# Kernel tuning notes

Hardware: AMD Instinct MI355X
Metric: run time of the kernel (lower is better)

The kernel has to match this reference:

```python
import jax, jax.numpy as jnp
import numpy as np

H = 64
VOCAB = 64
NUM_PAIRS = 6
ENERGY_THRESHOLD = 0.4
LN_EPS = 1e-5


def setup_inputs() -> dict:
    key = jax.random.key(0)
    ks = jax.random.split(key, 16)
    B, L = 256, 2048
    s = 0.05
    return {
        "x": jax.random.randint(ks[0], (B, L), 0, VOCAB),
        "embed": jax.random.normal(ks[1], (VOCAB, H), jnp.float32) * s,
        "W1": jax.random.normal(ks[2], (2 * H, H), jnp.float32) * s,
        "b1": jnp.zeros((2 * H,), jnp.float32),
        "W2": jax.random.normal(ks[3], (H, 2 * H), jnp.float32) * s,
        "b2": jnp.zeros((H,), jnp.float32),
        "ln_g": jnp.ones((H,), jnp.float32),
        "ln_b": jnp.zeros((H,), jnp.float32),
        "Wk": jax.random.normal(ks[4], (H, H), jnp.float32) * s,
        "Wv": jax.random.normal(ks[5], (H, H), jnp.float32) * s,
        "Wq": jax.random.normal(ks[6], (H, H), jnp.float32) * s,
        "Wr": jax.random.normal(ks[7], (H, H), jnp.float32) * s,
        "alpha": jnp.float32(0.5),
        "Wout": jax.random.normal(ks[8], (VOCAB, H), jnp.float32) * s,
        "bout": jnp.zeros((VOCAB,), jnp.float32),
    }


def _layernorm(x, g, b):
    mu = jnp.mean(x, axis=-1, keepdims=True)
    var = jnp.var(x, axis=-1, keepdims=True)
    return (x - mu) * jax.lax.rsqrt(var + LN_EPS) * g + b


def _encoder(x, embed, W1, b1, W2, b2, ln_g, ln_b):
    h = embed[x]                                  # [B, L, H]
    ff = jax.nn.relu(h @ W1.T + b1) @ W2.T + b2   # [B, L, H]
    return _layernorm(h + ff, ln_g, ln_b)


def _forward(x, embed, W1, b1, W2, b2, ln_g, ln_b, Wk, Wv, Wq, Wr, alpha, Wout, bout):
    h = _encoder(x, embed, W1, b1, W2, b2, ln_g, ln_b)  # [B, L, H]
    B, L, _ = h.shape

    def step(M, h_t):  # M: [B, H, H], h_t: [B, H]
        k = h_t @ Wk.T
        k = k / jnp.maximum(jnp.linalg.norm(k, axis=-1, keepdims=True), 1e-12)
        v = h_t @ Wv.T
        pred = jnp.einsum("bij,bj->bi", M, k)
        delta = v - pred
        gate = (jnp.linalg.norm(delta, axis=-1) >
                ENERGY_THRESHOLD * jnp.linalg.norm(v, axis=-1)).astype(M.dtype)
        M = M + gate[:, None, None] * delta[:, :, None] * k[:, None, :]
        return M, None

    M0 = jnp.zeros((B, H, H), h.dtype)
    M, _ = jax.lax.scan(step, M0, jnp.swapaxes(h, 0, 1))  # scan over L

    q = h[:, -1, :] @ Wq.T                 # [B, H]
    slots = jnp.swapaxes(M, 1, 2)          # [B, H, H]
    k_s = min(NUM_PAIRS + 2, H)
    norms = jnp.linalg.norm(slots, axis=-1)            # [B, H]
    _, topk_i = jax.lax.top_k(norms, k_s)              # [B, k_s]
    sel = jnp.take_along_axis(slots, topk_i[:, :, None], axis=1)  # [B, k_s, H]
    q_r = q @ Wr.T
    attn = jax.nn.softmax(jnp.einsum("bkh,bh->bk", sel, q_r) / jnp.sqrt(jnp.float32(H)), axis=-1)
    retro_ctx = jnp.einsum("bk,bkh->bh", attn, sel)    # [B, H]
    m_ctx = jnp.einsum("bij,bj->bi", M, q)             # [B, H]
    a = jax.nn.sigmoid(alpha)
    mixed = jax.nn.relu(a * retro_ctx + (1.0 - a) * m_ctx)
    return mixed @ Wout.T + bout           # [B, VOCAB]


def reference(x, embed, W1, b1, W2, b2, ln_g, ln_b, Wk, Wv, Wq, Wr, alpha, Wout, bout):
    return _forward(x, embed, W1, b1, W2, b2, ln_g, ln_b, Wk, Wv, Wq, Wr, alpha, Wout, bout)
```

## Files before the change

kernel.cpp:

```cpp
#include <hip/hip_runtime.h>
#include <math.h>

#define H 64
#define VOCABN 64
#define LSEQ 2048
#define LN_EPS 1e-5f

template <int CTRL>
__device__ __forceinline__ float dpp_add(float x) {
  return x + __int_as_float(__builtin_amdgcn_update_dpp(
      0, __float_as_int(x), CTRL, 0xF, 0xF, true));
}

__device__ __forceinline__ float wave_allsum(float x) {
  x = dpp_add<0xB1>(x);
  x = dpp_add<0x4E>(x);
  x = dpp_add<0x141>(x);
  x = dpp_add<0x140>(x);
  x += __shfl_xor(x, 16, 64);
  x += __shfl_xor(x, 32, 64);
  return x;
}

__device__ __forceinline__ float reduce_to_lane63(float x) {
  x = dpp_add<0x111>(x);
  x = dpp_add<0x112>(x);
  x = dpp_add<0x114>(x);
  x = dpp_add<0x118>(x);
  x = dpp_add<0x142>(x);
  x = dpp_add<0x143>(x);
  return x;
}

__global__ __launch_bounds__(64) void tables_kernel(
    const float* __restrict__ embed, const float* __restrict__ W1, const float* __restrict__ b1,
    const float* __restrict__ W2, const float* __restrict__ b2,
    const float* __restrict__ ln_g, const float* __restrict__ ln_b,
    const float* __restrict__ Wk, const float* __restrict__ Wv,
    float* __restrict__ Htab, float* __restrict__ Ktab, float* __restrict__ Vtab,
    float* __restrict__ nvtab)
{
  __shared__ float hs[H];
  __shared__ float ff1[2 * H];
  __shared__ float lns[H];
  const int c = blockIdx.x;
  const int i = threadIdx.x;

  float e = embed[c * H + i];
  hs[i] = e;
  __syncthreads();

  float r1 = b1[i], r2 = b1[i + H];
  for (int j = 0; j < H; ++j) {
    float hj = hs[j];
    r1 = fmaf(W1[i * H + j], hj, r1);
    r2 = fmaf(W1[(i + H) * H + j], hj, r2);
  }
  ff1[i]     = fmaxf(r1, 0.f);
  ff1[i + H] = fmaxf(r2, 0.f);
  __syncthreads();

  float o = b2[i];
  for (int m = 0; m < 2 * H; ++m) o = fmaf(W2[i * 2 * H + m], ff1[m], o);
  float y = e + o;

  float mu  = wave_allsum(y) * (1.f / H);
  float d   = y - mu;
  float var = wave_allsum(d * d) * (1.f / H);
  float ln  = d * (1.f / sqrtf(var + LN_EPS)) * ln_g[i] + ln_b[i];
  lns[i] = ln;
  __syncthreads();
  Htab[c * H + i] = ln;

  float k = 0.f, v = 0.f;
  for (int j = 0; j < H; ++j) {
    float lj = lns[j];
    k = fmaf(Wk[i * H + j], lj, k);
    v = fmaf(Wv[i * H + j], lj, v);
  }
  float nk = sqrtf(wave_allsum(k * k));
  Ktab[c * H + i] = k / fmaxf(nk, 1e-12f);
  Vtab[c * H + i] = v;
  float nv = sqrtf(wave_allsum(v * v));
  if (i == 0) nvtab[c] = 0.4f * nv;
}

__global__ __launch_bounds__(256, 1) void scan_kernel(
    const int* __restrict__ x, const float* __restrict__ Htab,
    const float* __restrict__ Ktab, const float* __restrict__ Vtab,
    const float* __restrict__ nvtab,
    const float* __restrict__ Wq, const float* __restrict__ Wr,
    const float* __restrict__ alpha, const float* __restrict__ Wout,
    const float* __restrict__ bout, float* __restrict__ out)
{
  __shared__ float4 Kl4[VOCABN * H / 4];
  __shared__ float4 Vl4[VOCABN * H / 4];
  __shared__ float4 Gl4[VOCABN * H / 4];
  __shared__ float4 Rl4[VOCABN * H / 4];
  __shared__ int4   xl4[LSEQ / 4];
  __shared__ float  thl[VOCABN];
  __shared__ float  hbuf[H];
  __shared__ float  qbuf[H];
  __shared__ float  mbuf[H];
  float* Kl = (float*)Kl4;
  float* Vl = (float*)Vl4;
  float* Gl = (float*)Gl4;
  float* Rl = (float*)Rl4;
  int*   xl = (int*)xl4;

  const int b    = blockIdx.x;
  const int tid  = threadIdx.x;
  const int lane = tid & 63;
  const int wid  = tid >> 6;

  {
    const float4* Kg = (const float4*)Ktab;
    const float4* Vg = (const float4*)Vtab;
    for (int q = tid; q < VOCABN * H / 4; q += 256) {
      float4 vq = Vg[q];
      Kl4[q] = Kg[q]; Vl4[q] = vq; Rl4[q] = vq;
    }
    const int4* xg = (const int4*)(x + b * LSEQ);
    for (int q = tid; q < LSEQ / 4; q += 256) xl4[q] = xg[q];
    if (tid < VOCABN) thl[tid] = nvtab[tid];
  }
  __syncthreads();

  {
    float4 kr[16];
#pragma unroll
    for (int q = 0; q < 16; ++q) kr[q] = Kl4[lane * 16 + q];
    for (int r = 0; r < 16; ++r) {
      const int c2 = wid * 16 + r;
      const float4* kp2 = (const float4*)(Kl + c2 * H);
      float a0 = 0.f, a1 = 0.f, a2 = 0.f, a3 = 0.f;
#pragma unroll
      for (int q = 0; q < 16; ++q) {
        float4 kq = kp2[q];
        a0 = fmaf(kr[q].x, kq.x, a0);
        a1 = fmaf(kr[q].y, kq.y, a1);
        a2 = fmaf(kr[q].z, kq.z, a2);
        a3 = fmaf(kr[q].w, kq.w, a3);
      }
      Gl[c2 * H + lane] = (a0 + a1) + (a2 + a3);
    }
  }
  __syncthreads();

  float4 Mw[4];
#pragma unroll
  for (int q = 0; q < 4; ++q) Mw[q] = make_float4(0.f, 0.f, 0.f, 0.f);

  int   c0 = xl[0], c1 = xl[1];
  float rv  = Rl[c0 * H + lane];
  float rvn = Rl[c1 * H + lane];
  float th0 = thl[c0], th1 = thl[c1];

  for (int t = 0; t < LSEQ; ++t) {
    const int ix2 = (t + 2 < LSEQ) ? t + 2 : LSEQ - 1;
    const int c2  = xl[ix2];
    float rb2  = Rl[c2 * H + lane];
    float th2v = thl[c2];
    float g01  = Gl[c0 * H + c1];
    float g02  = Gl[c0 * H + c2];

    float nd2 = reduce_to_lane63(rv * rv);
    float nds = sqrtf(__int_as_float(__builtin_amdgcn_readlane(__float_as_int(nd2), 63)));
    float thu = __int_as_float(__builtin_amdgcn_readfirstlane(__float_as_int(th0)));

    if (nds > thu) {
      const float delta = rv;
      rvn = fmaf(-g01, delta, rvn);
      rb2 = fmaf(-g02, delta, rb2);
      __syncthreads();
      const float4* gp = ((const float4*)(Gl + c0 * H)) + wid * 4;
      float4 ga = gp[0], gb = gp[1], gc = gp[2], gd = gp[3];
      float gs[16] = {ga.x, ga.y, ga.z, ga.w, gb.x, gb.y, gb.z, gb.w,
                      gc.x, gc.y, gc.z, gc.w, gd.x, gd.y, gd.z, gd.w};
#pragma unroll
      for (int r = 0; r < 16; ++r) {
        const int cc = wid * 16 + r;
        Rl[cc * H + lane] = fmaf(-gs[r], delta, Rl[cc * H + lane]);
      }
      const float4* kp = ((const float4*)(Kl + c0 * H)) + wid * 4;
#pragma unroll
      for (int q = 0; q < 4; ++q) {
        float4 k4 = kp[q];
        Mw[q].x = fmaf(delta, k4.x, Mw[q].x);
        Mw[q].y = fmaf(delta, k4.y, Mw[q].y);
        Mw[q].z = fmaf(delta, k4.z, Mw[q].z);
        Mw[q].w = fmaf(delta, k4.w, Mw[q].w);
      }
      __syncthreads();
    }
    rv = rvn; rvn = rb2; c0 = c1; c1 = c2; th0 = th1; th1 = th2v;
  }

  __syncthreads();
#pragma unroll
  for (int r = 0; r < 4; ++r) {
    const int jb = wid * 16 + r * 4;
    float4 m = Mw[r];
    Vl[(jb + 0) * H + lane] = m.x;
    Vl[(jb + 1) * H + lane] = m.y;
    Vl[(jb + 2) * H + lane] = m.z;
    Vl[(jb + 3) * H + lane] = m.w;
    Kl[lane * H + jb + 0] = m.x;
    Kl[lane * H + jb + 1] = m.y;
    Kl[lane * H + jb + 2] = m.z;
    Kl[lane * H + jb + 3] = m.w;
  }
  __syncthreads();

  if (wid == 0) {
    const int clast = xl[LSEQ - 1];
    hbuf[lane] = Htab[clast * H + lane];

    float qi = 0.f;
    for (int j = 0; j < H; ++j) qi = fmaf(Wq[lane * H + j], hbuf[j], qi);
    qbuf[lane] = qi;

    float qri = 0.f;
    for (int j = 0; j < H; ++j) qri = fmaf(Wr[lane * H + j], qbuf[j], qri);

    float n2 = 0.f;
    for (int i2 = 0; i2 < H; ++i2) { float m = Kl[i2 * H + lane]; n2 = fmaf(m, m, n2); }

    const int KS = 8;
    int idxs[KS];
    float nloc = n2;
#pragma unroll
    for (int k = 0; k < KS; ++k) {
      float v = nloc; int idx = lane;
#pragma unroll
      for (int s = 1; s < 64; s <<= 1) {
        float ov = __shfl_xor(v, s, 64);
        int   oi = __shfl_xor(idx, s, 64);
        if (ov > v || (ov == v && oi < idx)) { v = ov; idx = oi; }
      }
      idxs[k] = idx;
      if (lane == idx) nloc = -1.f;
    }

    float sel[KS], lg[KS];
#pragma unroll
    for (int k = 0; k < KS; ++k) {
      float s = Vl[idxs[k] * H + lane];
      sel[k] = s;
      lg[k] = wave_allsum(s * qri) * 0.125f;
    }
    float lmax = lg[0];
#pragma unroll
    for (int k = 1; k < KS; ++k) lmax = fmaxf(lmax, lg[k]);
    float esum = 0.f, retro = 0.f;
#pragma unroll
    for (int k = 0; k < KS; ++k) {
      float e = expf(lg[k] - lmax);
      esum += e;
      retro = fmaf(e, sel[k], retro);
    }
    retro /= esum;

    float mc = 0.f;
    for (int j = 0; j < H; ++j) mc = fmaf(Vl[j * H + lane], qbuf[j], mc);

    float a = 1.f / (1.f + expf(-alpha[0]));
    float mixed = fmaxf(fmaf(a, retro, (1.f - a) * mc), 0.f);
    mbuf[lane] = mixed;

    float oo = bout[lane];
    for (int i2 = 0; i2 < H; ++i2) oo = fmaf(Wout[lane * H + i2], mbuf[i2], oo);
    out[b * VOCABN + lane] = oo;
  }
}

extern "C" void kernel_launch(void* const* d_in, const int* in_sizes, int n_in,
                              void* d_out, int out_size, void* d_ws, size_t ws_size,
                              hipStream_t stream) {
  const int*   x     = (const int*)d_in[0];
  const float* embed = (const float*)d_in[1];
  const float* W1    = (const float*)d_in[2];
  const float* b1    = (const float*)d_in[3];
  const float* W2    = (const float*)d_in[4];
  const float* b2    = (const float*)d_in[5];
  const float* ln_g  = (const float*)d_in[6];
  const float* ln_b  = (const float*)d_in[7];
  const float* Wk    = (const float*)d_in[8];
  const float* Wv    = (const float*)d_in[9];
  const float* Wq    = (const float*)d_in[10];
  const float* Wr    = (const float*)d_in[11];
  const float* alpha = (const float*)d_in[12];
  const float* Wout  = (const float*)d_in[13];
  const float* bout  = (const float*)d_in[14];
  float* out = (float*)d_out;

  const int B = in_sizes[0] / LSEQ;

  float* ws    = (float*)d_ws;
  float* Htab  = ws;
  float* Ktab  = ws + 4096;
  float* Vtab  = ws + 8192;
  float* nvtab = ws + 12288;

  tables_kernel<<<VOCABN, 64, 0, stream>>>(embed, W1, b1, W2, b2, ln_g, ln_b,
                                           Wk, Wv, Htab, Ktab, Vtab, nvtab);
  scan_kernel<<<B, 256, 0, stream>>>(x, Htab, Ktab, Vtab, nvtab,
                                     Wq, Wr, alpha, Wout, bout, out);
}
```

Before: 561.9 us.

## Double-buffer residual table to drop a barrier and precompute next-step norms

Splits the shared residual table into two ping-pong buffers, so the gated update writes into the next buffer while reading the current one. This removes the barrier that used to come before the update. The norm of the next step's residual is now computed ahead of time: speculatively for the rejected case, and recomputed after the update for the accepted case. This takes the wave reduction off the critical path at the branch. It costs an extra 16 KB of LDS and one extra wave reduction per step.

```diff
diff --git a/kernel.cpp b/kernel.cpp
--- a/kernel.cpp
+++ b/kernel.cpp
@@ -30,6 +30,11 @@
   x = dpp_add<0x142>(x);
   x = dpp_add<0x143>(x);
   return x;
+}
+
+__device__ __forceinline__ float wave_norm63(float x) {
+  float nd2 = reduce_to_lane63(x * x);
+  return sqrtf(__int_as_float(__builtin_amdgcn_readlane(__float_as_int(nd2), 63)));
 }
 
 __global__ __launch_bounds__(64) void tables_kernel(
@@ -96,7 +101,8 @@
   __shared__ float4 Kl4[VOCABN * H / 4];
   __shared__ float4 Vl4[VOCABN * H / 4];
   __shared__ float4 Gl4[VOCABN * H / 4];
-  __shared__ float4 Rl4[VOCABN * H / 4];
+  __shared__ float4 Ra4[VOCABN * H / 4];
+  __shared__ float4 Rb4[VOCABN * H / 4];
   __shared__ int4   xl4[LSEQ / 4];
   __shared__ float  thl[VOCABN];
   __shared__ float  hbuf[H];
@@ -105,7 +111,6 @@
   float* Kl = (float*)Kl4;
   float* Vl = (float*)Vl4;
   float* Gl = (float*)Gl4;
-  float* Rl = (float*)Rl4;
   int*   xl = (int*)xl4;
 
   const int b    = blockIdx.x;
@@ -118,7 +123,7 @@
     const float4* Vg = (const float4*)Vtab;
     for (int q = tid; q < VOCABN * H / 4; q += 256) {
       float4 vq = Vg[q];
-      Kl4[q] = Kg[q]; Vl4[q] = vq; Rl4[q] = vq;
+      Kl4[q] = Kg[q]; Vl4[q] = vq; Ra4[q] = vq;
     }
     const int4* xg = (const int4*)(x + b * LSEQ);
     for (int q = tid; q < LSEQ / 4; q += 256) xl4[q] = xg[q];
@@ -151,28 +156,33 @@
 #pragma unroll
   for (int q = 0; q < 4; ++q) Mw[q] = make_float4(0.f, 0.f, 0.f, 0.f);
 
+  float* cur = (float*)Ra4;
+  float* nxt = (float*)Rb4;
+
   int   c0 = xl[0], c1 = xl[1];
-  float rv  = Rl[c0 * H + lane];
-  float rvn = Rl[c1 * H + lane];
-  float th0 = thl[c0], th1 = thl[c1];
+  float rv   = cur[c0 * H + lane];
+  float rvn  = cur[c1 * H + lane];
+  float th0  = thl[c0], th1 = thl[c1];
+  float nds0 = wave_norm63(rv);
 
   for (int t = 0; t < LSEQ; ++t) {
     const int ix2 = (t + 2 < LSEQ) ? t + 2 : LSEQ - 1;
     const int c2  = xl[ix2];
-    float rb2  = Rl[c2 * H + lane];
+    float rb2  = cur[c2 * H + lane];
     float th2v = thl[c2];
     float g01  = Gl[c0 * H + c1];
     float g02  = Gl[c0 * H + c2];
 
-    float nd2 = reduce_to_lane63(rv * rv);
-    float nds = sqrtf(__int_as_float(__builtin_amdgcn_readlane(__float_as_int(nd2), 63)));
+    float nds_rej = wave_norm63(rvn);
+
     float thu = __int_as_float(__builtin_amdgcn_readfirstlane(__float_as_int(th0)));
-
-    if (nds > thu) {
+    float nds_next;
+
+    if (nds0 > thu) {
       const float delta = rv;
       rvn = fmaf(-g01, delta, rvn);
       rb2 = fmaf(-g02, delta, rb2);
-      __syncthreads();
+      nds_next = wave_norm63(rvn);
       const float4* gp = ((const float4*)(Gl + c0 * H)) + wid * 4;
       float4 ga = gp[0], gb = gp[1], gc = gp[2], gd = gp[3];
       float gs[16] = {ga.x, ga.y, ga.z, ga.w, gb.x, gb.y, gb.z, gb.w,
@@ -180,7 +190,7 @@
 #pragma unroll
       for (int r = 0; r < 16; ++r) {
         const int cc = wid * 16 + r;
-        Rl[cc * H + lane] = fmaf(-gs[r], delta, Rl[cc * H + lane]);
+        nxt[cc * H + lane] = fmaf(-gs[r], delta, cur[cc * H + lane]);
       }
       const float4* kp = ((const float4*)(Kl + c0 * H)) + wid * 4;
 #pragma unroll
@@ -192,8 +202,13 @@
         Mw[q].w = fmaf(delta, k4.w, Mw[q].w);
       }
       __syncthreads();
-    }
-    rv = rvn; rvn = rb2; c0 = c1; c1 = c2; th0 = th1; th1 = th2v;
+      float* tmp = cur; cur = nxt; nxt = tmp;
+    } else {
+      nds_next = nds_rej;
+    }
+
+    rv = rvn; rvn = rb2; nds0 = nds_next;
+    c0 = c1; c1 = c2; th0 = th1; th1 = th2v;
   }
 
   __syncthreads();
```

Result: slower. 723.3 us (+28.7%).

## Double block to 512 threads and prefetch scan operands one step ahead

Applied to the files above, without the earlier changes.

The scan block grows from 4 to 8 waves, so each wave updates 8 residual rows and 8 memory columns per step instead of 16. The per-step work is also rearranged: the norm of the next residuals, the Gram coefficients and the K/G row slices for the next token are computed at the end of the previous iteration, and the norms are recomputed only when an update changes those residuals. The aim is to shorten the serial critical path between gate decisions. In exchange, each step's barriers now wait on twice as many waves and there are extra LDS reads, and the epilogue and any later code must still be right for the new wave mapping.

```diff
diff --git a/kernel.cpp b/kernel.cpp
--- a/kernel.cpp
+++ b/kernel.cpp
@@ -30,6 +30,11 @@
   x = dpp_add<0x142>(x);
   x = dpp_add<0x143>(x);
   return x;
+}
+
+__device__ __forceinline__ float wave_norm63(float x) {
+  float nd2 = reduce_to_lane63(x * x);
+  return sqrtf(__int_as_float(__builtin_amdgcn_readlane(__float_as_int(nd2), 63)));
 }
 
 __global__ __launch_bounds__(64) void tables_kernel(
@@ -85,7 +90,7 @@
   if (i == 0) nvtab[c] = 0.4f * nv;
 }
 
-__global__ __launch_bounds__(256, 1) void scan_kernel(
+__global__ __launch_bounds__(512, 1) void scan_kernel(
     const int* __restrict__ x, const float* __restrict__ Htab,
     const float* __restrict__ Ktab, const float* __restrict__ Vtab,
     const float* __restrict__ nvtab,
@@ -116,12 +121,12 @@
   {
     const float4* Kg = (const float4*)Ktab;
     const float4* Vg = (const float4*)Vtab;
-    for (int q = tid; q < VOCABN * H / 4; q += 256) {
+    for (int q = tid; q < VOCABN * H / 4; q += 512) {
       float4 vq = Vg[q];
       Kl4[q] = Kg[q]; Vl4[q] = vq; Rl4[q] = vq;
     }
     const int4* xg = (const int4*)(x + b * LSEQ);
-    for (int q = tid; q < LSEQ / 4; q += 256) xl4[q] = xg[q];
+    for (int q = tid; q < LSEQ / 4; q += 512) xl4[q] = xg[q];
     if (tid < VOCABN) thl[tid] = nvtab[tid];
   }
   __syncthreads();
@@ -130,8 +135,8 @@
     float4 kr[16];
 #pragma unroll
     for (int q = 0; q < 16; ++q) kr[q] = Kl4[lane * 16 + q];
-    for (int r = 0; r < 16; ++r) {
-      const int c2 = wid * 16 + r;
+    for (int r = 0; r < 8; ++r) {
+      const int c2 = wid * 8 + r;
       const float4* kp2 = (const float4*)(Kl + c2 * H);
       float a0 = 0.f, a1 = 0.f, a2 = 0.f, a3 = 0.f;
 #pragma unroll
@@ -147,59 +152,76 @@
   }
   __syncthreads();
 
-  float4 Mw[4];
-#pragma unroll
-  for (int q = 0; q < 4; ++q) Mw[q] = make_float4(0.f, 0.f, 0.f, 0.f);
-
-  int   c0 = xl[0], c1 = xl[1];
+  float4 Mw[2];
+  Mw[0] = make_float4(0.f, 0.f, 0.f, 0.f);
+  Mw[1] = make_float4(0.f, 0.f, 0.f, 0.f);
+
+  int   c0 = xl[0], c1 = xl[1], c2 = xl[2];
   float rv  = Rl[c0 * H + lane];
   float rvn = Rl[c1 * H + lane];
-  float th0 = thl[c0], th1 = thl[c1];
+  float rb2 = Rl[c2 * H + lane];
+  float th0 = thl[c0], th1 = thl[c1], th2 = thl[c2];
+  float nds0 = wave_norm63(rv);
+  float nds1 = wave_norm63(rvn);
+  float nds2 = wave_norm63(rb2);
+  float g01 = Gl[c0 * H + c1];
+  float g02 = Gl[c0 * H + c2];
+  float4 gp0 = ((const float4*)(Gl + c0 * H))[wid * 2 + 0];
+  float4 gp1 = ((const float4*)(Gl + c0 * H))[wid * 2 + 1];
+  float4 kp0 = ((const float4*)(Kl + c0 * H))[wid * 2 + 0];
+  float4 kp1 = ((const float4*)(Kl + c0 * H))[wid * 2 + 1];
 
   for (int t = 0; t < LSEQ; ++t) {
-    const int ix2 = (t + 2 < LSEQ) ? t + 2 : LSEQ - 1;
-    const int c2  = xl[ix2];
-    float rb2  = Rl[c2 * H + lane];
-    float th2v = thl[c2];
-    float g01  = Gl[c0 * H + c1];
-    float g02  = Gl[c0 * H + c2];
-
-    float nd2 = reduce_to_lane63(rv * rv);
-    float nds = sqrtf(__int_as_float(__builtin_amdgcn_readlane(__float_as_int(nd2), 63)));
+    const int i3 = (t + 3 < LSEQ) ? t + 3 : LSEQ - 1;
+    const int c3 = xl[i3];
+    const float th3 = thl[c3];
+
     float thu = __int_as_float(__builtin_amdgcn_readfirstlane(__float_as_int(th0)));
 
-    if (nds > thu) {
+    if (nds0 > thu) {
       const float delta = rv;
       rvn = fmaf(-g01, delta, rvn);
       rb2 = fmaf(-g02, delta, rb2);
+      nds1 = wave_norm63(rvn);
+      nds2 = wave_norm63(rb2);
       __syncthreads();
-      const float4* gp = ((const float4*)(Gl + c0 * H)) + wid * 4;
-      float4 ga = gp[0], gb = gp[1], gc = gp[2], gd = gp[3];
-      float gs[16] = {ga.x, ga.y, ga.z, ga.w, gb.x, gb.y, gb.z, gb.w,
-                      gc.x, gc.y, gc.z, gc.w, gd.x, gd.y, gd.z, gd.w};
-#pragma unroll
-      for (int r = 0; r < 16; ++r) {
-        const int cc = wid * 16 + r;
+      float gs[8] = {gp0.x, gp0.y, gp0.z, gp0.w, gp1.x, gp1.y, gp1.z, gp1.w};
+#pragma unroll
+      for (int r = 0; r < 8; ++r) {
+        const int cc = wid * 8 + r;
         Rl[cc * H + lane] = fmaf(-gs[r], delta, Rl[cc * H + lane]);
       }
-      const float4* kp = ((const float4*)(Kl + c0 * H)) + wid * 4;
-#pragma unroll
-      for (int q = 0; q < 4; ++q) {
-        float4 k4 = kp[q];
-        Mw[q].x = fmaf(delta, k4.x, Mw[q].x);
-        Mw[q].y = fmaf(delta, k4.y, Mw[q].y);
-        Mw[q].z = fmaf(delta, k4.z, Mw[q].z);
-        Mw[q].w = fmaf(delta, k4.w, Mw[q].w);
-      }
+      Mw[0].x = fmaf(delta, kp0.x, Mw[0].x);
+      Mw[0].y = fmaf(delta, kp0.y, Mw[0].y);
+      Mw[0].z = fmaf(delta, kp0.z, Mw[0].z);
+      Mw[0].w = fmaf(delta, kp0.w, Mw[0].w);
+      Mw[1].x = fmaf(delta, kp1.x, Mw[1].x);
+      Mw[1].y = fmaf(delta, kp1.y, Mw[1].y);
+      Mw[1].z = fmaf(delta, kp1.z, Mw[1].z);
+      Mw[1].w = fmaf(delta, kp1.w, Mw[1].w);
       __syncthreads();
     }
-    rv = rvn; rvn = rb2; c0 = c1; c1 = c2; th0 = th1; th1 = th2v;
-  }
-
-  __syncthreads();
-#pragma unroll
-  for (int r = 0; r < 4; ++r) {
-    const int jb = wid * 16 + r * 4;
+
+    float rb3  = Rl[c3 * H + lane];
+    float nds3 = wave_norm63(rb3);
+    float g01n = Gl[c1 * H + c2];
+    float g02n = Gl[c1 * H + c3];
+    gp0 = ((const float4*)(Gl + c1 * H))[wid * 2 + 0];
+    gp1 = ((const float4*)(Gl + c1 * H))[wid * 2 + 1];
+    kp0 = ((const float4*)(Kl + c1 * H))[wid * 2 + 0];
+    kp1 = ((const float4*)(Kl + c1 * H))[wid * 2 + 1];
+
+    rv = rvn; rvn = rb2; rb2 = rb3;
+    nds0 = nds1; nds1 = nds2; nds2 = nds3;
+    c0 = c1; c1 = c2; c2 = c3;
+    th0 = th1; th1 = th2; th2 = th3;
+    g01 = g01n; g02 = g02n;
+  }
+
+  __syncthreads();
+#pragma unroll
+  for (int r = 0; r < 2; ++r) {
+    const int jb = wid * 8 + r * 4;
     float4 m = Mw[r];
     Vl[(jb + 0) * H + lane] = m.x;
     Vl[(jb + 1) * H + lane] = m.y;
@@ -304,6 +326,6 @@
 
   tables_kernel<<<VOCABN, 64, 0, stream>>>(embed, W1, b1, W2, b2, ln_g, ln_b,
                                            Wk, Wv, Htab, Ktab, Vtab, nvtab);
-  scan_kernel<<<B, 256, 0, stream>>>(x, Htab, Ktab, Vtab, nvtab,
+  scan_kernel<<<B, 512, 0, stream>>>(x, Htab, Ktab, Vtab, nvtab,
                                      Wq, Wr, alpha, Wout, bout, out);
 }
```

Result: slower. 840.2 us (+49.5%).

## Deepen scan lookahead to four steps with precomputed Gram sequence and norms

Applied to the files above, without the earlier changes.

Precomputes per-timestep Gram entries (G[x_t, x_{t+1..4}]) and thresholds into shared arrays before the scan. The loop now keeps four residual rows in registers with their norms computed ahead, and prefetches the next token's G and K slices. This takes the wave reduction and shared-memory loads off the serial dependency chain of each step. In exchange it uses more shared memory (and reuses the aux buffer for M at the end) and more registers, and adds extra norm recomputation when the gate fires.

```diff
diff --git a/kernel.cpp b/kernel.cpp
--- a/kernel.cpp
+++ b/kernel.cpp
@@ -30,6 +30,15 @@
   x = dpp_add<0x142>(x);
   x = dpp_add<0x143>(x);
   return x;
+}
+
+__device__ __forceinline__ float rdlf(float v, int lane) {
+  return __int_as_float(__builtin_amdgcn_readlane(__float_as_int(v), lane));
+}
+
+__device__ __forceinline__ float wave_norm63(float x) {
+  float nd2 = reduce_to_lane63(x * x);
+  return sqrtf(rdlf(nd2, 63));
 }
 
 __global__ __launch_bounds__(64) void tables_kernel(
@@ -94,19 +103,21 @@
     const float* __restrict__ bout, float* __restrict__ out)
 {
   __shared__ float4 Kl4[VOCABN * H / 4];
-  __shared__ float4 Vl4[VOCABN * H / 4];
-  __shared__ float4 Gl4[VOCABN * H / 4];
+  __shared__ float  Gl[VOCABN * H];
   __shared__ float4 Rl4[VOCABN * H / 4];
-  __shared__ int4   xl4[LSEQ / 4];
+  __shared__ int    xl[LSEQ];
+  __shared__ float  thseq[LSEQ];
+  __shared__ float  aux[4 * LSEQ];
   __shared__ float  thl[VOCABN];
   __shared__ float  hbuf[H];
   __shared__ float  qbuf[H];
   __shared__ float  mbuf[H];
-  float* Kl = (float*)Kl4;
-  float* Vl = (float*)Vl4;
-  float* Gl = (float*)Gl4;
-  float* Rl = (float*)Rl4;
-  int*   xl = (int*)xl4;
+  float* Kl  = (float*)Kl4;
+  float* Rl  = (float*)Rl4;
+  float* gs1 = aux;
+  float* gs2 = aux + LSEQ;
+  float* gs3 = aux + 2 * LSEQ;
+  float* gs4 = aux + 3 * LSEQ;
 
   const int b    = blockIdx.x;
   const int tid  = threadIdx.x;
@@ -116,11 +127,9 @@
   {
     const float4* Kg = (const float4*)Ktab;
     const float4* Vg = (const float4*)Vtab;
-    for (int q = tid; q < VOCABN * H / 4; q += 256) {
-      float4 vq = Vg[q];
-      Kl4[q] = Kg[q]; Vl4[q] = vq; Rl4[q] = vq;
-    }
+    for (int q = tid; q < VOCABN * H / 4; q += 256) { Kl4[q] = Kg[q]; Rl4[q] = Vg[q]; }
     const int4* xg = (const int4*)(x + b * LSEQ);
+    int4* xl4 = (int4*)xl;
     for (int q = tid; q < LSEQ / 4; q += 256) xl4[q] = xg[q];
     if (tid < VOCABN) thl[tid] = nvtab[tid];
   }
@@ -147,64 +156,111 @@
   }
   __syncthreads();
 
+  for (int t = tid; t < LSEQ; t += 256) {
+    const int a  = xl[t];
+    const int i1 = (t + 1 < LSEQ) ? t + 1 : LSEQ - 1;
+    const int i2 = (t + 2 < LSEQ) ? t + 2 : LSEQ - 1;
+    const int i3 = (t + 3 < LSEQ) ? t + 3 : LSEQ - 1;
+    const int i4 = (t + 4 < LSEQ) ? t + 4 : LSEQ - 1;
+    gs1[t] = Gl[a * H + xl[i1]];
+    gs2[t] = Gl[a * H + xl[i2]];
+    gs3[t] = Gl[a * H + xl[i3]];
+    gs4[t] = Gl[a * H + xl[i4]];
+    thseq[t] = thl[a];
+  }
+  __syncthreads();
+
   float4 Mw[4];
 #pragma unroll
   for (int q = 0; q < 4; ++q) Mw[q] = make_float4(0.f, 0.f, 0.f, 0.f);
 
-  int   c0 = xl[0], c1 = xl[1];
-  float rv  = Rl[c0 * H + lane];
-  float rvn = Rl[c1 * H + lane];
-  float th0 = thl[c0], th1 = thl[c1];
+  int c0 = xl[0], c1 = xl[1], c2 = xl[2], c3 = xl[3];
+  float r0 = Rl[c0 * H + lane];
+  float r1 = Rl[c1 * H + lane];
+  float r2 = Rl[c2 * H + lane];
+  float r3 = Rl[c3 * H + lane];
+  float n0 = wave_norm63(r0);
+  float n1 = wave_norm63(r1);
+  float n2 = wave_norm63(r2);
+  float th0 = thseq[0];
+  float g1 = gs1[0], g2 = gs2[0], g3 = gs3[0], g4 = gs4[0];
+  float4 gA, gB, gC, gD, kA, kB, kC, kD;
+  {
+    const float4* gpp = ((const float4*)(Gl + c0 * H)) + wid * 4;
+    const float4* kpp = ((const float4*)(Kl + c0 * H)) + wid * 4;
+    gA = gpp[0]; gB = gpp[1]; gC = gpp[2]; gD = gpp[3];
+    kA = kpp[0]; kB = kpp[1]; kC = kpp[2]; kD = kpp[3];
+  }
 
   for (int t = 0; t < LSEQ; ++t) {
-    const int ix2 = (t + 2 < LSEQ) ? t + 2 : LSEQ - 1;
-    const int c2  = xl[ix2];
-    float rb2  = Rl[c2 * H + lane];
-    float th2v = thl[c2];
-    float g01  = Gl[c0 * H + c1];
-    float g02  = Gl[c0 * H + c2];
-
-    float nd2 = reduce_to_lane63(rv * rv);
-    float nds = sqrtf(__int_as_float(__builtin_amdgcn_readlane(__float_as_int(nd2), 63)));
-    float thu = __int_as_float(__builtin_amdgcn_readfirstlane(__float_as_int(th0)));
-
-    if (nds > thu) {
-      const float delta = rv;
-      rvn = fmaf(-g01, delta, rvn);
-      rb2 = fmaf(-g02, delta, rb2);
+    const int i4x = (t + 4 < LSEQ) ? t + 4 : LSEQ - 1;
+    const int i1x = (t + 1 < LSEQ) ? t + 1 : LSEQ - 1;
+    const int c4  = xl[i4x];
+    float r4 = Rl[c4 * H + lane];
+    float n3 = wave_norm63(r3);
+    float thn = thseq[i1x];
+    float gn1 = gs1[i1x], gn2 = gs2[i1x], gn3 = gs3[i1x], gn4 = gs4[i1x];
+
+    const float thu = __int_as_float(__builtin_amdgcn_readfirstlane(__float_as_int(th0)));
+
+    if (n0 > thu) {
+      const float delta = r0;
+      r1 = fmaf(-g1, delta, r1);
+      r2 = fmaf(-g2, delta, r2);
+      r3 = fmaf(-g3, delta, r3);
+      n1 = wave_norm63(r1);
+      n2 = wave_norm63(r2);
+      n3 = wave_norm63(r3);
       __syncthreads();
-      const float4* gp = ((const float4*)(Gl + c0 * H)) + wid * 4;
-      float4 ga = gp[0], gb = gp[1], gc = gp[2], gd = gp[3];
-      float gs[16] = {ga.x, ga.y, ga.z, ga.w, gb.x, gb.y, gb.z, gb.w,
-                      gc.x, gc.y, gc.z, gc.w, gd.x, gd.y, gd.z, gd.w};
+      float gsl[16] = {gA.x, gA.y, gA.z, gA.w, gB.x, gB.y, gB.z, gB.w,
+                       gC.x, gC.y, gC.z, gC.w, gD.x, gD.y, gD.z, gD.w};
 #pragma unroll
       for (int r = 0; r < 16; ++r) {
         const int cc = wid * 16 + r;
-        Rl[cc * H + lane] = fmaf(-gs[r], delta, Rl[cc * H + lane]);
+        Rl[cc * H + lane] = fmaf(-gsl[r], delta, Rl[cc * H + lane]);
       }
-      const float4* kp = ((const float4*)(Kl + c0 * H)) + wid * 4;
-#pragma unroll
-      for (int q = 0; q < 4; ++q) {
-        float4 k4 = kp[q];
-        Mw[q].x = fmaf(delta, k4.x, Mw[q].x);
-        Mw[q].y = fmaf(delta, k4.y, Mw[q].y);
-        Mw[q].z = fmaf(delta, k4.z, Mw[q].z);
-        Mw[q].w = fmaf(delta, k4.w, Mw[q].w);
-      }
+      Mw[0].x = fmaf(delta, kA.x, Mw[0].x);
+      Mw[0].y = fmaf(delta, kA.y, Mw[0].y);
+      Mw[0].z = fmaf(delta, kA.z, Mw[0].z);
+      Mw[0].w = fmaf(delta, kA.w, Mw[0].w);
+      Mw[1].x = fmaf(delta, kB.x, Mw[1].x);
+      Mw[1].y = fmaf(delta, kB.y, Mw[1].y);
+      Mw[1].z = fmaf(delta, kB.z, Mw[1].z);
+      Mw[1].w = fmaf(delta, kB.w, Mw[1].w);
+      Mw[2].x = fmaf(delta, kC.x, Mw[2].x);
+      Mw[2].y = fmaf(delta, kC.y, Mw[2].y);
+      Mw[2].z = fmaf(delta, kC.z, Mw[2].z);
+      Mw[2].w = fmaf(delta, kC.w, Mw[2].w);
+      Mw[3].x = fmaf(delta, kD.x, Mw[3].x);
+      Mw[3].y = fmaf(delta, kD.y, Mw[3].y);
+      Mw[3].z = fmaf(delta, kD.z, Mw[3].z);
+      Mw[3].w = fmaf(delta, kD.w, Mw[3].w);
       __syncthreads();
-    }
-    rv = rvn; rvn = rb2; c0 = c1; c1 = c2; th0 = th1; th1 = th2v;
-  }
-
-  __syncthreads();
+      r4 = fmaf(-g4, delta, r4);
+    }
+
+    {
+      const float4* gpn = ((const float4*)(Gl + c1 * H)) + wid * 4;
+      const float4* kpn = ((const float4*)(Kl + c1 * H)) + wid * 4;
+      gA = gpn[0]; gB = gpn[1]; gC = gpn[2]; gD = gpn[3];
+      kA = kpn[0]; kB = kpn[1]; kC = kpn[2]; kD = kpn[3];
+    }
+    r0 = r1; r1 = r2; r2 = r3; r3 = r4;
+    n0 = n1; n1 = n2; n2 = n3;
+    c0 = c1; c1 = c2; c2 = c3; c3 = c4;
+    th0 = thn; g1 = gn1; g2 = gn2; g3 = gn3; g4 = gn4;
+  }
+
+  __syncthreads();
+  float* Mt = aux;
 #pragma unroll
   for (int r = 0; r < 4; ++r) {
     const int jb = wid * 16 + r * 4;
     float4 m = Mw[r];
-    Vl[(jb + 0) * H + lane] = m.x;
-    Vl[(jb + 1) * H + lane] = m.y;
-    Vl[(jb + 2) * H + lane] = m.z;
-    Vl[(jb + 3) * H + lane] = m.w;
+    Mt[(jb + 0) * H + lane] = m.x;
+    Mt[(jb + 1) * H + lane] = m.y;
+    Mt[(jb + 2) * H + lane] = m.z;
+    Mt[(jb + 3) * H + lane] = m.w;
     Kl[lane * H + jb + 0] = m.x;
     Kl[lane * H + jb + 1] = m.y;
     Kl[lane * H + jb + 2] = m.z;
@@ -223,12 +279,12 @@
     float qri = 0.f;
     for (int j = 0; j < H; ++j) qri = fmaf(Wr[lane * H + j], qbuf[j], qri);
 
-    float n2 = 0.f;
-    for (int i2 = 0; i2 < H; ++i2) { float m = Kl[i2 * H + lane]; n2 = fmaf(m, m, n2); }
+    float n2r = 0.f;
+    for (int i2 = 0; i2 < H; ++i2) { float m = Kl[i2 * H + lane]; n2r = fmaf(m, m, n2r); }
 
     const int KS = 8;
     int idxs[KS];
-    float nloc = n2;
+    float nloc = n2r;
 #pragma unroll
     for (int k = 0; k < KS; ++k) {
       float v = nloc; int idx = lane;
@@ -245,7 +301,7 @@
     float sel[KS], lg[KS];
 #pragma unroll
     for (int k = 0; k < KS; ++k) {
-      float s = Vl[idxs[k] * H + lane];
+      float s = Mt[idxs[k] * H + lane];
       sel[k] = s;
       lg[k] = wave_allsum(s * qri) * 0.125f;
     }
@@ -262,7 +318,7 @@
     retro /= esum;
 
     float mc = 0.f;
-    for (int j = 0; j < H; ++j) mc = fmaf(Vl[j * H + lane], qbuf[j], mc);
+    for (int j = 0; j < H; ++j) mc = fmaf(Mt[j * H + lane], qbuf[j], mc);
 
     float a = 1.f / (1.f + expf(-alpha[0]));
     float mixed = fmaxf(fmaf(a, retro, (1.f - a) * mc), 0.f);
```

Result: slower. 776.3 us (+38.1%).
